# Kernel optimization log

Measured on AMD Instinct MI355X. Metric: run time of the kernel, lower is better.

Reference implementation:

```python
import jax, jax.numpy as jnp
import numpy as np

N = 50000   # nodes
E = 500000  # edges
IN = 128    # input_dim
H = 8       # num_heads
D = 32      # hidden_dim (per head)
HD = H * D  # 256
PERM = 100
B = 64      # graphs in batch
C = 10      # num_classes
SLOPE = 0.2 # DGL GATConv leaky_relu default


def setup_inputs() -> dict:
    key = jax.random.key(0)
    ks = jax.random.split(key, 16)
    def glorot(k, shape, fan_in):
        return jax.random.normal(k, shape, dtype=jnp.float32) / np.sqrt(fan_in)
    return {
        "h": jax.random.normal(ks[0], (N, IN), dtype=jnp.float32),
        "perm_features": jax.random.normal(ks[1], (B, PERM), dtype=jnp.float32),
        "W1": glorot(ks[2], (IN, HD), IN),
        "al1": glorot(ks[3], (H, D), D),
        "ar1": glorot(ks[4], (H, D), D),
        "b1": jnp.zeros((HD,), jnp.float32),
        "W2": glorot(ks[5], (HD, HD), HD),
        "al2": glorot(ks[6], (H, D), D),
        "ar2": glorot(ks[7], (H, D), D),
        "b2": jnp.zeros((HD,), jnp.float32),
        "Wc": glorot(ks[8], (HD + PERM, C), HD + PERM),
        "bc": jnp.zeros((C,), jnp.float32),
        "src": jax.random.randint(ks[9], (E,), 0, N, dtype=jnp.int32),
        "dst": jax.random.randint(ks[10], (E,), 0, N, dtype=jnp.int32),
        "graph_ids": jnp.sort(jax.random.randint(ks[11], (N,), 0, B, dtype=jnp.int32)),
    }


def _leaky_relu(x):
    return jnp.where(x > 0, x, SLOPE * x)


def gat_conv(h, W, al, ar, b, src, dst):
    """DGL GATConv: multi-head edge attention + segment softmax + scatter-agg."""
    n = h.shape[0]
    z = (h @ W).reshape(n, H, D)                       # [N,H,D]
    el = jnp.einsum('nhd,hd->nh', z, al)               # [N,H]
    er = jnp.einsum('nhd,hd->nh', z, ar)               # [N,H]
    e = _leaky_relu(el[src] + er[dst])                 # [E,H]
    # segment softmax over incoming edges of each dst node
    m = jax.ops.segment_max(e, dst, num_segments=n)    # [N,H]
    m = jnp.where(jnp.isfinite(m), m, 0.0)             # empty segments -> 0
    w = jnp.exp(e - m[dst])                            # [E,H]
    s = jax.ops.segment_sum(w, dst, num_segments=n)    # [N,H]
    alpha = w / s[dst]                                 # [E,H]
    # weighted scatter-aggregate of source messages
    out = jax.ops.segment_sum(alpha[:, :, None] * z[src], dst, num_segments=n)
    return out + b.reshape(1, H, D)                    # [N,H,D]


def reference(h, perm_features, W1, al1, ar1, b1, W2, al2, ar2, b2, Wc, bc,
              src, dst, graph_ids):
    h1 = jax.nn.relu(gat_conv(h, W1, al1, ar1, b1, src, dst)).reshape(N, HD)
    h2 = gat_conv(h1, W2, al2, ar2, b2, src, dst).reshape(N, HD)
    # dgl.mean_nodes: per-graph mean over nodes
    sums = jax.ops.segment_sum(h2, graph_ids, num_segments=B)            # [B,HD]
    cnts = jax.ops.segment_sum(jnp.ones((N, 1), h2.dtype), graph_ids,
                               num_segments=B)                            # [B,1]
    hg = sums / jnp.maximum(cnts, 1.0)
    combined = jnp.concatenate([hg, perm_features], axis=1)               # [B,HD+PERM]
    return combined @ Wc + bc                                             # [B,C]
```

## Files before the change

### kernel.cpp

```cpp
#include <hip/hip_runtime.h>
#include <hip/hip_bf16.h>

#define NN 50000
#define NE 500000
#define INDIM 128
#define NH 8
#define DH 32
#define HD 256
#define NPERM 100
#define NB_G 64
#define NC 10
#define SLOPE 0.2f
#define BCAP 64

typedef short bf16x8 __attribute__((ext_vector_type(8)));
typedef float f32x4 __attribute__((ext_vector_type(4)));

__device__ inline float bf2f(unsigned short u) {
    union { unsigned int i; float f; } x; x.i = ((unsigned int)u) << 16; return x.f;
}
__device__ inline unsigned short f2bf(float f) {
    __hip_bfloat16 h = __float2bfloat16(f);
    return *reinterpret_cast<unsigned short*>(&h);
}


#define NB_CNT ((NN + 255) / 256)

__global__ __launch_bounds__(256) void prep_kernel(
    int* __restrict__ counts,
    const float* __restrict__ W1, const float* __restrict__ W2,
    __hip_bfloat16* __restrict__ Wt1, __hip_bfloat16* __restrict__ Wt2,
    float* __restrict__ hg)
{
    int b = blockIdx.x;
    int c = threadIdx.x;
    if (b < NB_CNT) {
        int i = b * 256 + c;
        if (i < NN) counts[i] = 0;
    } else {
        int bb = b - NB_CNT;
        if (bb < INDIM) {
            Wt1[(size_t)c * INDIM + bb] = __float2bfloat16(W1[(size_t)bb * HD + c]);
        } else {
            int k = bb - INDIM;
            Wt2[(size_t)c * HD + k] = __float2bfloat16(W2[(size_t)k * HD + c]);
        }
        if (bb < NB_G) hg[bb * HD + c] = 0.f;
    }
}


template<int IS_F32>
__global__ __launch_bounds__(256) void gemm_mfma_kernel(
    const void* __restrict__ Xv, const __hip_bfloat16* __restrict__ Wt,
    const float* __restrict__ al, const float* __restrict__ ar,
    __hip_bfloat16* __restrict__ zb, float* __restrict__ el, float* __restrict__ er,
    int nrows, int K, int gemm_nblocks,
    const int* __restrict__ dstv, const int* __restrict__ srcv,
    int* __restrict__ counts, int* __restrict__ bucket, int ne)
{
    __shared__ __attribute__((aligned(16))) unsigned short Xs[64 * 64];
    int t = threadIdx.x;

    if ((int)blockIdx.x >= gemm_nblocks) {
        int e = ((int)blockIdx.x - gemm_nblocks) * 256 + t;
        if (e < ne) {
            int d = dstv[e];
            int p = atomicAdd(&counts[d], 1);
            if (p < BCAP) bucket[(size_t)d * BCAP + p] = srcv[e];
        }
        return;
    }

    int l = t & 63;
    int wc = t >> 6;
    int nb = blockIdx.x * 64;
    int wcb = wc * 64;
    int lg = l >> 4;
    int lr = l & 15;

    const short* Wt16 = (const short*)Wt;

    f32x4 acc[4][4];
#pragma unroll
    for (int rb = 0; rb < 4; ++rb)
#pragma unroll
        for (int cf = 0; cf < 4; ++cf) acc[rb][cf] = (f32x4){0.f, 0.f, 0.f, 0.f};

    int srow = t >> 2;
    int sslot = t & 3;
    int g_row0 = t >> 3;
    int g_row1 = (t + 256) >> 3;
    int g_p    = t & 7;

    for (int kc = 0; kc < K; kc += 64) {
        bf16x8 b[2][4];
#pragma unroll
        for (int kh = 0; kh < 2; ++kh)
#pragma unroll
            for (int cf = 0; cf < 4; ++cf) {
                int col = wcb + cf * 16 + lr;
                b[kh][cf] = *(const bf16x8*)&Wt16[(size_t)col * K + kc + kh * 32 + lg * 8];
            }

        if (IS_F32) {
            bf16x8 xv0 = {0,0,0,0,0,0,0,0}, xv1 = {0,0,0,0,0,0,0,0};
            int gr = nb + srow;
            if (gr < nrows) {
                const float* Xf = (const float*)Xv;
                const float* p = &Xf[(size_t)gr * K + kc];
                float4 xa = *(const float4*)&p[sslot * 8];
                float4 xb = *(const float4*)&p[sslot * 8 + 4];
                float4 xc = *(const float4*)&p[(sslot + 4) * 8];
                float4 xd = *(const float4*)&p[(sslot + 4) * 8 + 4];
                xv0[0] = (short)f2bf(xa.x); xv0[1] = (short)f2bf(xa.y);
                xv0[2] = (short)f2bf(xa.z); xv0[3] = (short)f2bf(xa.w);
                xv0[4] = (short)f2bf(xb.x); xv0[5] = (short)f2bf(xb.y);
                xv0[6] = (short)f2bf(xb.z); xv0[7] = (short)f2bf(xb.w);
                xv1[0] = (short)f2bf(xc.x); xv1[1] = (short)f2bf(xc.y);
                xv1[2] = (short)f2bf(xc.z); xv1[3] = (short)f2bf(xc.w);
                xv1[4] = (short)f2bf(xd.x); xv1[5] = (short)f2bf(xd.y);
                xv1[6] = (short)f2bf(xd.z); xv1[7] = (short)f2bf(xd.w);
            }
            __syncthreads();
            *(bf16x8*)&Xs[srow * 64 + ((sslot ^ (srow & 7)) * 8)] = xv0;
            *(bf16x8*)&Xs[srow * 64 + (((sslot + 4) ^ (srow & 7)) * 8)] = xv1;
            __syncthreads();
        } else {
            const short* X16 = (const short*)Xv;
            __syncthreads();
            {
                int q0 = g_p ^ (g_row0 & 7);
                int q1 = g_p ^ (g_row1 & 7);
                const short* ga0 = &X16[(size_t)(nb + g_row0) * K + kc + q0 * 8];
                const short* ga1 = &X16[(size_t)(nb + g_row1) * K + kc + q1 * 8];
                __builtin_amdgcn_global_load_lds(
                    (const __attribute__((address_space(1))) void*)ga0,
                    (__attribute__((address_space(3))) void*)((char*)Xs + t * 16), 16, 0, 0);
                __builtin_amdgcn_global_load_lds(
                    (const __attribute__((address_space(1))) void*)ga1,
                    (__attribute__((address_space(3))) void*)((char*)Xs + (t + 256) * 16), 16, 0, 0);
            }
            __syncthreads();
        }

        bf16x8 a[2][4];
#pragma unroll
        for (int kh = 0; kh < 2; ++kh)
#pragma unroll
            for (int rb = 0; rb < 4; ++rb) {
                int row = rb * 16 + lr;
                int slot = (kh * 4 + lg) ^ (row & 7);
                a[kh][rb] = *(const bf16x8*)&Xs[row * 64 + slot * 8];
            }
#pragma unroll
        for (int kh = 0; kh < 2; ++kh)
#pragma unroll
            for (int rb = 0; rb < 4; ++rb)
#pragma unroll
                for (int cf = 0; cf < 4; ++cf)
                    acc[rb][cf] = __builtin_amdgcn_mfma_f32_16x16x32_bf16(a[kh][rb], b[kh][cf], acc[rb][cf], 0, 0, 0);
    }

    float al_c[4], ar_c[4];
#pragma unroll
    for (int cf = 0; cf < 4; ++cf) {
        al_c[cf] = al[wcb + cf * 16 + lr];
        ar_c[cf] = ar[wcb + cf * 16 + lr];
    }

    unsigned short* zu = (unsigned short*)zb;
#pragma unroll
    for (int rb = 0; rb < 4; ++rb) {
        int rbase = nb + rb * 16 + lg * 4;
#pragma unroll
        for (int j = 0; j < 4; ++j) {
            int r = rbase + j;
            if (r < nrows) {
#pragma unroll
                for (int cf = 0; cf < 4; ++cf)
                    zu[(size_t)r * HD + wcb + cf * 16 + lr] = f2bf(acc[rb][cf][j]);
            }
        }
        float p0[4], p1[4], q0[4], q1[4];
#pragma unroll
        for (int j = 0; j < 4; ++j) {
            p0[j] = acc[rb][0][j] * al_c[0] + acc[rb][1][j] * al_c[1];
            p1[j] = acc[rb][2][j] * al_c[2] + acc[rb][3][j] * al_c[3];
            q0[j] = acc[rb][0][j] * ar_c[0] + acc[rb][1][j] * ar_c[1];
            q1[j] = acc[rb][2][j] * ar_c[2] + acc[rb][3][j] * ar_c[3];
        }
#pragma unroll
        for (int m = 1; m < 16; m <<= 1) {
#pragma unroll
            for (int j = 0; j < 4; ++j) {
                p0[j] += __shfl_xor(p0[j], m);
                p1[j] += __shfl_xor(p1[j], m);
                q0[j] += __shfl_xor(q0[j], m);
                q1[j] += __shfl_xor(q1[j], m);
            }
        }
        if (lr == 0) {
#pragma unroll
            for (int j = 0; j < 4; ++j) {
                int r = rbase + j;
                if (r < nrows) {
                    el[(size_t)r * NH + 2 * wc]     = p0[j];
                    el[(size_t)r * NH + 2 * wc + 1] = p1[j];
                    er[(size_t)r * NH + 2 * wc]     = q0[j];
                    er[(size_t)r * NH + 2 * wc + 1] = q1[j];
                }
            }
        }
    }
}


__global__ __launch_bounds__(256) void agg_kernel(
    const __hip_bfloat16* __restrict__ zb, const float* __restrict__ el, const float* __restrict__ er,
    const float* __restrict__ bias, const int* __restrict__ counts,
    const int* __restrict__ bucket, __hip_bfloat16* __restrict__ out, int nrows, int do_relu)
{
    int wid = (blockIdx.x * 256 + threadIdx.x) >> 6;
    int l = threadIdx.x & 63;
    if (wid >= nrows) return;
    int n = wid;
    int K = counts[n];
    if (K > BCAP) K = BCAP;
    const int* srcs = &bucket[(size_t)n * BCAP];
    const unsigned short* zu = (const unsigned short*)zb;

    int es = l >> 4;
    int li = l & 15;
    int hh = li >> 1;
    float ern = er[(size_t)n * NH + hh];
    int c0 = li * 16;

    float num[16];
#pragma unroll
    for (int j = 0; j < 16; ++j) num[j] = 0.f;
    float den = 0.f;

    for (int kb = 0; kb < K; kb += 4) {
        int k = kb + es;
        if (k < K) {
            int s = srcs[k];
            float v = el[(size_t)s * NH + hh] + ern;
            v = v > 0.f ? v : SLOPE * v;
            float w = __expf(v);
            den += w;
            const unsigned short* zr = &zu[(size_t)s * HD + c0];
            bf16x8 z0 = *(const bf16x8*)&zr[0];
            bf16x8 z1 = *(const bf16x8*)&zr[8];
#pragma unroll
            for (int j = 0; j < 8; ++j) {
                num[j]     += w * bf2f((unsigned short)z0[j]);
                num[8 + j] += w * bf2f((unsigned short)z1[j]);
            }
        }
    }

    den += __shfl_xor(den, 16);
    den += __shfl_xor(den, 32);
#pragma unroll
    for (int j = 0; j < 16; ++j) {
        num[j] += __shfl_xor(num[j], 16);
        num[j] += __shfl_xor(num[j], 32);
    }

    if (es == 0) {
        float inv = (K > 0) ? 1.0f / den : 0.f;
        unsigned short* op = (unsigned short*)out;
        float4 bva = *(const float4*)&bias[c0];
        float4 bvb = *(const float4*)&bias[c0 + 4];
        float4 bvc = *(const float4*)&bias[c0 + 8];
        float4 bvd = *(const float4*)&bias[c0 + 12];
        float bb[16] = {bva.x, bva.y, bva.z, bva.w, bvb.x, bvb.y, bvb.z, bvb.w,
                        bvc.x, bvc.y, bvc.z, bvc.w, bvd.x, bvd.y, bvd.z, bvd.w};
        bf16x8 o0, o1;
#pragma unroll
        for (int j = 0; j < 8; ++j) {
            float v0 = num[j] * inv + bb[j];
            float v1 = num[8 + j] * inv + bb[8 + j];
            if (do_relu) { v0 = fmaxf(v0, 0.f); v1 = fmaxf(v1, 0.f); }
            o0[j] = (short)f2bf(v0);
            o1[j] = (short)f2bf(v1);
        }
        *(bf16x8*)&op[(size_t)n * HD + c0] = o0;
        *(bf16x8*)&op[(size_t)n * HD + c0 + 8] = o1;
    }
}


__global__ __launch_bounds__(256) void graph_sum_kernel(
    const __hip_bfloat16* __restrict__ h2, const int* __restrict__ gids,
    float* __restrict__ hg)
{
    int c = threadIdx.x;
    int n0 = blockIdx.x * 64;
    int n1 = n0 + 64;
    if (n0 >= NN) return;
    if (n1 > NN) n1 = NN;
    const unsigned short* hu = (const unsigned short*)h2;
    float acc = 0.f;
    int cur = gids[n0];
    for (int n = n0; n < n1; ++n) {
        int g = gids[n];
        if (g != cur) {
            atomicAdd(&hg[cur * HD + c], acc);
            acc = 0.f;
            cur = g;
        }
        acc += bf2f(hu[(size_t)n * HD + c]);
    }
    atomicAdd(&hg[cur * HD + c], acc);
}

__global__ void classifier_kernel(const float* __restrict__ hg, const float* __restrict__ perm,
                                  const float* __restrict__ Wc, const float* __restrict__ bc,
                                  const int* __restrict__ gids, float* __restrict__ out) {
    int g = blockIdx.x;
    int c = threadIdx.x;
    if (c >= NC) return;
    int lo = 0, hi = NN;
    while (lo < hi) { int mid = (lo + hi) >> 1; if (gids[mid] < g) lo = mid + 1; else hi = mid; }
    int s0 = lo;
    lo = 0; hi = NN;
    while (lo < hi) { int mid = (lo + hi) >> 1; if (gids[mid] < g + 1) lo = mid + 1; else hi = mid; }
    float cnt = fmaxf((float)(lo - s0), 1.0f);
    float inv = 1.0f / cnt;
    float sg = 0.f;
    for (int k = 0; k < HD; ++k) sg += hg[g * HD + k] * Wc[k * NC + c];
    float s = bc[c] + sg * inv;
    for (int k = 0; k < NPERM; ++k) s += perm[g * NPERM + k] * Wc[(HD + k) * NC + c];
    out[g * NC + c] = s;
}


extern "C" void kernel_launch(void* const* d_in, const int* in_sizes, int n_in,
                              void* d_out, int out_size, void* d_ws, size_t ws_size,
                              hipStream_t stream) {
    const float* h    = (const float*)d_in[0];
    const float* perm = (const float*)d_in[1];
    const float* W1   = (const float*)d_in[2];
    const float* al1  = (const float*)d_in[3];
    const float* ar1  = (const float*)d_in[4];
    const float* b1   = (const float*)d_in[5];
    const float* W2   = (const float*)d_in[6];
    const float* al2  = (const float*)d_in[7];
    const float* ar2  = (const float*)d_in[8];
    const float* b2   = (const float*)d_in[9];
    const float* Wc   = (const float*)d_in[10];
    const float* bc   = (const float*)d_in[11];
    const int* src    = (const int*)d_in[12];
    const int* dst    = (const int*)d_in[13];
    const int* gids   = (const int*)d_in[14];
    float* out = (float*)d_out;

    __hip_bfloat16* zb  = (__hip_bfloat16*)d_ws;
    __hip_bfloat16* h1b = zb + (size_t)NN * HD;
    __hip_bfloat16* Wt1 = h1b + (size_t)NN * HD;
    __hip_bfloat16* Wt2 = Wt1 + (size_t)HD * INDIM;
    float* el = (float*)(Wt2 + (size_t)HD * HD);
    float* er = el + (size_t)NN * NH;
    float* hg = er + (size_t)NN * NH;
    int* counts = (int*)(hg + NB_G * HD);
    int* bucket = counts + NN;

    int nblocks_e = (NE + 255) / 256;
    int gemm_blocks = (NN + 63) / 64;
    int wave_node_blocks = (NN * 64 + 255) / 256;

    prep_kernel<<<NB_CNT + INDIM + HD, 256, 0, stream>>>(counts, W1, W2, Wt1, Wt2, hg);

    gemm_mfma_kernel<1><<<gemm_blocks + nblocks_e, 256, 0, stream>>>(
        h, Wt1, al1, ar1, zb, el, er, NN, INDIM,
        gemm_blocks, dst, src, counts, bucket, NE);
    agg_kernel<<<wave_node_blocks, 256, 0, stream>>>(zb, el, er, b1, counts, bucket, h1b, NN, 1);
    gemm_mfma_kernel<0><<<gemm_blocks, 256, 0, stream>>>(
        h1b, Wt2, al2, ar2, zb, el, er, NN, HD,
        gemm_blocks, nullptr, nullptr, nullptr, nullptr, 0);
    agg_kernel<<<wave_node_blocks, 256, 0, stream>>>(zb, el, er, b2, counts, bucket, h1b, NN, 0);

    graph_sum_kernel<<<(NN + 63) / 64, 256, 0, stream>>>(h1b, gids, hg);
    classifier_kernel<<<NB_G, 64, 0, stream>>>(hg, perm, Wc, bc, gids, out);
}
```

Baseline: 212.1 us.

## Stage full-K input tile in LDS once and template GEMM on K

The GEMM kernel now takes K as a template parameter and loads the whole 64xK input tile into shared memory in one pass before the MFMA loop. This replaces the per-64-chunk loop that needed two barriers per iteration. It removes repeated synchronisation and lets the compiler fully unroll the K loop, including the weight loads. The cost is more LDS per block (up to 32KB for K=256) and more registers from unrolling, which may lower occupancy.

```diff
diff --git a/kernel.cpp b/kernel.cpp
--- a/kernel.cpp
+++ b/kernel.cpp
@@ -51,16 +51,16 @@
 }
 
 
-template<int IS_F32>
+template<int KVAL, int IS_F32>
 __global__ __launch_bounds__(256) void gemm_mfma_kernel(
     const void* __restrict__ Xv, const __hip_bfloat16* __restrict__ Wt,
     const float* __restrict__ al, const float* __restrict__ ar,
     __hip_bfloat16* __restrict__ zb, float* __restrict__ el, float* __restrict__ er,
-    int nrows, int K, int gemm_nblocks,
+    int nrows, int gemm_nblocks,
     const int* __restrict__ dstv, const int* __restrict__ srcv,
     int* __restrict__ counts, int* __restrict__ bucket, int ne)
 {
-    __shared__ __attribute__((aligned(16))) unsigned short Xs[64 * 64];
+    __shared__ __attribute__((aligned(16))) unsigned short Xs[64 * KVAL];
     int t = threadIdx.x;
 
     if ((int)blockIdx.x >= gemm_nblocks) {
@@ -81,6 +81,43 @@
     int lr = l & 15;
 
     const short* Wt16 = (const short*)Wt;
+    constexpr int NSLOT = KVAL / 8;
+    constexpr int NKK = KVAL / 32;
+
+    if (IS_F32) {
+        const float* Xf = (const float*)Xv;
+        int row = t >> 2;
+        int gr = nb + row;
+#pragma unroll
+        for (int i = 0; i < NSLOT / 4; ++i) {
+            int j = (t & 3) + 4 * i;
+            bf16x8 xv = {0, 0, 0, 0, 0, 0, 0, 0};
+            if (gr < nrows) {
+                const float* p = &Xf[(size_t)gr * KVAL + j * 8];
+                float4 xa = *(const float4*)&p[0];
+                float4 xb = *(const float4*)&p[4];
+                xv[0] = (short)f2bf(xa.x); xv[1] = (short)f2bf(xa.y);
+                xv[2] = (short)f2bf(xa.z); xv[3] = (short)f2bf(xa.w);
+                xv[4] = (short)f2bf(xb.x); xv[5] = (short)f2bf(xb.y);
+                xv[6] = (short)f2bf(xb.z); xv[7] = (short)f2bf(xb.w);
+            }
+            *(bf16x8*)&Xs[row * KVAL + ((j ^ (row & 7)) * 8)] = xv;
+        }
+    } else {
+        const short* X16 = (const short*)Xv;
+#pragma unroll
+        for (int i = 0; i < (64 * NSLOT) / 256; ++i) {
+            int c = t + i * 256;
+            int row = c / NSLOT;
+            int p = c % NSLOT;
+            int q = p ^ (row & 7);
+            const short* ga = &X16[(size_t)(nb + row) * KVAL + q * 8];
+            __builtin_amdgcn_global_load_lds(
+                (const __attribute__((address_space(1))) void*)ga,
+                (__attribute__((address_space(3))) void*)((char*)Xs + (size_t)c * 16), 16, 0, 0);
+        }
+    }
+    __syncthreads();
 
     f32x4 acc[4][4];
 #pragma unroll
@@ -88,79 +125,25 @@
 #pragma unroll
         for (int cf = 0; cf < 4; ++cf) acc[rb][cf] = (f32x4){0.f, 0.f, 0.f, 0.f};
 
-    int srow = t >> 2;
-    int sslot = t & 3;
-    int g_row0 = t >> 3;
-    int g_row1 = (t + 256) >> 3;
-    int g_p    = t & 7;
-
-    for (int kc = 0; kc < K; kc += 64) {
-        bf16x8 b[2][4];
-#pragma unroll
-        for (int kh = 0; kh < 2; ++kh)
-#pragma unroll
-            for (int cf = 0; cf < 4; ++cf) {
-                int col = wcb + cf * 16 + lr;
-                b[kh][cf] = *(const bf16x8*)&Wt16[(size_t)col * K + kc + kh * 32 + lg * 8];
-            }
-
-        if (IS_F32) {
-            bf16x8 xv0 = {0,0,0,0,0,0,0,0}, xv1 = {0,0,0,0,0,0,0,0};
-            int gr = nb + srow;
-            if (gr < nrows) {
-                const float* Xf = (const float*)Xv;
-                const float* p = &Xf[(size_t)gr * K + kc];
-                float4 xa = *(const float4*)&p[sslot * 8];
-                float4 xb = *(const float4*)&p[sslot * 8 + 4];
-                float4 xc = *(const float4*)&p[(sslot + 4) * 8];
-                float4 xd = *(const float4*)&p[(sslot + 4) * 8 + 4];
-                xv0[0] = (short)f2bf(xa.x); xv0[1] = (short)f2bf(xa.y);
-                xv0[2] = (short)f2bf(xa.z); xv0[3] = (short)f2bf(xa.w);
-                xv0[4] = (short)f2bf(xb.x); xv0[5] = (short)f2bf(xb.y);
-                xv0[6] = (short)f2bf(xb.z); xv0[7] = (short)f2bf(xb.w);
-                xv1[0] = (short)f2bf(xc.x); xv1[1] = (short)f2bf(xc.y);
-                xv1[2] = (short)f2bf(xc.z); xv1[3] = (short)f2bf(xc.w);
-                xv1[4] = (short)f2bf(xd.x); xv1[5] = (short)f2bf(xd.y);
-                xv1[6] = (short)f2bf(xd.z); xv1[7] = (short)f2bf(xd.w);
-            }
-            __syncthreads();
-            *(bf16x8*)&Xs[srow * 64 + ((sslot ^ (srow & 7)) * 8)] = xv0;
-            *(bf16x8*)&Xs[srow * 64 + (((sslot + 4) ^ (srow & 7)) * 8)] = xv1;
-            __syncthreads();
-        } else {
-            const short* X16 = (const short*)Xv;
-            __syncthreads();
-            {
-                int q0 = g_p ^ (g_row0 & 7);
-                int q1 = g_p ^ (g_row1 & 7);
-                const short* ga0 = &X16[(size_t)(nb + g_row0) * K + kc + q0 * 8];
-                const short* ga1 = &X16[(size_t)(nb + g_row1) * K + kc + q1 * 8];
-                __builtin_amdgcn_global_load_lds(
-                    (const __attribute__((address_space(1))) void*)ga0,
-                    (__attribute__((address_space(3))) void*)((char*)Xs + t * 16), 16, 0, 0);
-                __builtin_amdgcn_global_load_lds(
-                    (const __attribute__((address_space(1))) void*)ga1,
-                    (__attribute__((address_space(3))) void*)((char*)Xs + (t + 256) * 16), 16, 0, 0);
-            }
-            __syncthreads();
-        }
-
-        bf16x8 a[2][4];
-#pragma unroll
-        for (int kh = 0; kh < 2; ++kh)
-#pragma unroll
-            for (int rb = 0; rb < 4; ++rb) {
-                int row = rb * 16 + lr;
-                int slot = (kh * 4 + lg) ^ (row & 7);
-                a[kh][rb] = *(const bf16x8*)&Xs[row * 64 + slot * 8];
-            }
-#pragma unroll
-        for (int kh = 0; kh < 2; ++kh)
-#pragma unroll
-            for (int rb = 0; rb < 4; ++rb)
-#pragma unroll
-                for (int cf = 0; cf < 4; ++cf)
-                    acc[rb][cf] = __builtin_amdgcn_mfma_f32_16x16x32_bf16(a[kh][rb], b[kh][cf], acc[rb][cf], 0, 0, 0);
+#pragma unroll
+    for (int kk = 0; kk < NKK; ++kk) {
+        bf16x8 b[4], a[4];
+#pragma unroll
+        for (int cf = 0; cf < 4; ++cf) {
+            int col = wcb + cf * 16 + lr;
+            b[cf] = *(const bf16x8*)&Wt16[(size_t)col * KVAL + kk * 32 + lg * 8];
+        }
+#pragma unroll
+        for (int rb = 0; rb < 4; ++rb) {
+            int row = rb * 16 + lr;
+            int slot = (kk * 4 + lg) ^ (row & 7);
+            a[rb] = *(const bf16x8*)&Xs[row * KVAL + slot * 8];
+        }
+#pragma unroll
+        for (int rb = 0; rb < 4; ++rb)
+#pragma unroll
+            for (int cf = 0; cf < 4; ++cf)
+                acc[rb][cf] = __builtin_amdgcn_mfma_f32_16x16x32_bf16(a[rb], b[cf], acc[rb][cf], 0, 0, 0);
     }
 
     float al_c[4], ar_c[4];
@@ -374,12 +357,12 @@
 
     prep_kernel<<<NB_CNT + INDIM + HD, 256, 0, stream>>>(counts, W1, W2, Wt1, Wt2, hg);
 
-    gemm_mfma_kernel<1><<<gemm_blocks + nblocks_e, 256, 0, stream>>>(
-        h, Wt1, al1, ar1, zb, el, er, NN, INDIM,
+    gemm_mfma_kernel<INDIM, 1><<<gemm_blocks + nblocks_e, 256, 0, stream>>>(
+        h, Wt1, al1, ar1, zb, el, er, NN,
         gemm_blocks, dst, src, counts, bucket, NE);
     agg_kernel<<<wave_node_blocks, 256, 0, stream>>>(zb, el, er, b1, counts, bucket, h1b, NN, 1);
-    gemm_mfma_kernel<0><<<gemm_blocks, 256, 0, stream>>>(
-        h1b, Wt2, al2, ar2, zb, el, er, NN, HD,
+    gemm_mfma_kernel<HD, 0><<<gemm_blocks, 256, 0, stream>>>(
+        h1b, Wt2, al2, ar2, zb, el, er, NN,
         gemm_blocks, nullptr, nullptr, nullptr, nullptr, 0);
     agg_kernel<<<wave_node_blocks, 256, 0, stream>>>(zb, el, er, b2, counts, bucket, h1b, NN, 0);
 
```

Measured after the change: 211.9 us. About the same (-0.1%).
